# Kernel tuning notes

Hardware: AMD Instinct MI355X
Metric: run time of the kernel (lower is better)

Reference implementation:

```python
import jax, jax.numpy as jnp
import numpy as np

N = 16384      # total atoms (8 proteins x ~2048)
E = 524288     # N * max_neighbors(32)
B = 8          # graphs
F_IN = 26      # 20 residue types + 6 atom types
D = 128        # node_dim
H = 256        # hidden_dim
OUT = 64       # output_dim
L = 4          # n_layers
N_RBF = 16
CUTOFF = 10.0


def setup_inputs() -> dict:
    key = jax.random.key(0)
    ks = jax.random.split(key, 24)
    s = 0.05
    inp = {
        "positions": jax.random.normal(ks[0], (N, 3), jnp.float32) * 10.0,
        "node_features": jax.random.normal(ks[1], (N, F_IN), jnp.float32),
        "edge_index": jax.random.randint(ks[2], (2, E), 0, N, jnp.int32),
        "batch": jnp.sort(jax.random.randint(ks[3], (N,), 0, B, jnp.int32)),
        # node embedding MLP
        "emb_W1": jax.random.normal(ks[4], (F_IN, D), jnp.float32) * s,
        "emb_b1": jnp.zeros((D,), jnp.float32),
        "emb_W2": jax.random.normal(ks[5], (D, D), jnp.float32) * s,
        "emb_b2": jnp.zeros((D,), jnp.float32),
        # per-layer message MLP: [2D + n_rbf] -> H -> D
        "msg_W1": jax.random.normal(ks[6], (L, 2 * D + N_RBF, H), jnp.float32) * s,
        "msg_b1": jnp.zeros((L, H), jnp.float32),
        "msg_W2": jax.random.normal(ks[7], (L, H, D), jnp.float32) * s,
        "msg_b2": jnp.zeros((L, D), jnp.float32),
        # per-layer update MLP: [2D] -> H -> D (residual)
        "upd_W1": jax.random.normal(ks[8], (L, 2 * D, H), jnp.float32) * s,
        "upd_b1": jnp.zeros((L, H), jnp.float32),
        "upd_W2": jax.random.normal(ks[9], (L, H, D), jnp.float32) * s,
        "upd_b2": jnp.zeros((L, D), jnp.float32),
        # readout MLP: D -> H -> OUT
        "r_W1": jax.random.normal(ks[10], (D, H), jnp.float32) * s,
        "r_b1": jnp.zeros((H,), jnp.float32),
        "r_W2": jax.random.normal(ks[11], (H, OUT), jnp.float32) * s,
        "r_b2": jnp.zeros((OUT,), jnp.float32),
    }
    return inp


def _mlp2(x, W1, b1, W2, b2):
    return jax.nn.silu(x @ W1 + b1) @ W2 + b2


def _edge_rbf(positions, src, dst):
    rel = positions[dst] - positions[src]                      # (E,3)
    d = jnp.sqrt(jnp.sum(rel * rel, axis=-1) + 1e-12)          # (E,)
    centers = jnp.linspace(0.0, CUTOFF, N_RBF, dtype=positions.dtype)
    width = CUTOFF / N_RBF
    rbf = jnp.exp(-((d[:, None] - centers) ** 2) / (2.0 * width * width))  # (E,n_rbf)
    env = 0.5 * (jnp.cos(jnp.pi * d / CUTOFF) + 1.0) * (d < CUTOFF)        # cosine cutoff
    return rbf * env[:, None]


def reference(positions, node_features, edge_index, batch,
              emb_W1, emb_b1, emb_W2, emb_b2,
              msg_W1, msg_b1, msg_W2, msg_b2,
              upd_W1, upd_b1, upd_W2, upd_b2,
              r_W1, r_b1, r_W2, r_b2):
    src, dst = edge_index[0], edge_index[1]
    h = _mlp2(node_features, emb_W1, emb_b1, emb_W2, emb_b2)   # (N,D)
    ef = _edge_rbf(positions, src, dst)                        # (E,n_rbf)
    for i in range(L):
        m_in = jnp.concatenate([h[src], h[dst], ef], axis=-1)  # (E,2D+n_rbf)
        m = _mlp2(m_in, msg_W1[i], msg_b1[i], msg_W2[i], msg_b2[i])  # (E,D)
        agg = jax.ops.segment_sum(m, dst, num_segments=N)      # (N,D)
        u_in = jnp.concatenate([h, agg], axis=-1)              # (N,2D)
        h = h + _mlp2(u_in, upd_W1[i], upd_b1[i], upd_W2[i], upd_b2[i])
    # mean readout per graph
    counts = jax.ops.segment_sum(jnp.ones((N,), h.dtype), batch, num_segments=B)
    g = jax.ops.segment_sum(h, batch, num_segments=B) / jnp.maximum(counts, 1.0)[:, None]
    return _mlp2(g, r_W1, r_b1, r_W2, r_b2)                    # (B,OUT)
```

## Files before the change

### kernel.cpp

```cpp
#include <hip/hip_runtime.h>
#include <math.h>

#define NATOMS 16384
#define NEDGES 524288
#define NLAYERS 4
#define TE 64

typedef __bf16 bf16x8 __attribute__((ext_vector_type(8)));
typedef __bf16 bf16x4 __attribute__((ext_vector_type(4)));
typedef __bf16 bf16x2 __attribute__((ext_vector_type(2)));
typedef float f32x4 __attribute__((ext_vector_type(4)));

__device__ __forceinline__ float silu_f(float x) {
  return x * __builtin_amdgcn_rcpf(1.0f + __expf(-x));
}

__global__ __launch_bounds__(1024) void scan_kernel(
    const int* __restrict__ counts, int* __restrict__ cursor,
    float* __restrict__ degf)
{
  __shared__ int s_tot[1024];
  int tid = threadIdx.x;
  int v[16];
  {
    const int4* cp = (const int4*)(counts + tid * 16);
    int4 a = cp[0], b = cp[1], c = cp[2], d = cp[3];
    v[0]=a.x; v[1]=a.y; v[2]=a.z; v[3]=a.w;
    v[4]=b.x; v[5]=b.y; v[6]=b.z; v[7]=b.w;
    v[8]=c.x; v[9]=c.y; v[10]=c.z; v[11]=c.w;
    v[12]=d.x; v[13]=d.y; v[14]=d.z; v[15]=d.w;
  }
  int tot = 0;
  #pragma unroll
  for (int i = 0; i < 16; i++) tot += v[i];
  s_tot[tid] = tot;
  __syncthreads();
  for (int off = 1; off < 1024; off <<= 1) {
    int t = (tid >= off) ? s_tot[tid - off] : 0;
    __syncthreads();
    s_tot[tid] += t;
    __syncthreads();
  }
  int run = s_tot[tid] - tot;
  #pragma unroll
  for (int i = 0; i < 16; i++) {
    cursor[tid * 16 + i] = run;
    degf[tid * 16 + i] = (float)v[i];
    run += v[i];
  }
}

__global__ __launch_bounds__(256) void scatter_rbf_kernel(
    const int* __restrict__ src, const int* __restrict__ dst,
    int* __restrict__ cursor, const float* __restrict__ pos,
    int* __restrict__ esrc, int* __restrict__ edst,
    __bf16* __restrict__ efb)
{
  int e = blockIdx.x * 256 + threadIdx.x;
  int s = src[e], d = dst[e];
  int p = atomicAdd(&cursor[d], 1);
  esrc[p] = s;
  edst[p] = d;
  float dx = pos[d * 3 + 0] - pos[s * 3 + 0];
  float dy = pos[d * 3 + 1] - pos[s * 3 + 1];
  float dz = pos[d * 3 + 2] - pos[s * 3 + 2];
  float dist = sqrtf(dx * dx + dy * dy + dz * dz + 1e-12f);
  float env = (dist < 10.0f)
                  ? 0.5f * (cosf(3.14159265358979f * dist * 0.1f) + 1.0f)
                  : 0.0f;
  bf16x8 o0, o1;
  #pragma unroll
  for (int i = 0; i < 16; i++) {
    float c = (10.0f / 15.0f) * (float)i;
    float t = dist - c;
    float v = env * __expf(-t * t * 1.28f);
    if (i < 8) o0[i] = (__bf16)v; else o1[i - 8] = (__bf16)v;
  }
  *(bf16x8*)(efb + (size_t)p * 16 + 0) = o0;
  *(bf16x8*)(efb + (size_t)p * 16 + 8) = o1;
}

#define NB_PL   50
#define NB_PREP (NB_PL * NLAYERS)
#define NB_HIST (NEDGES / 256)
#define NB_EMB  (NATOMS / 32)

__global__ __launch_bounds__(256) void front_kernel(
    const float* __restrict__ mW1, const float* __restrict__ mW2,
    const float* __restrict__ uW1, const float* __restrict__ uW2,
    const float* __restrict__ mb2,
    __bf16* __restrict__ W1at, __bf16* __restrict__ W1bt,
    __bf16* __restrict__ B2c, __bf16* __restrict__ uW1ft,
    __bf16* __restrict__ uW2t, float* __restrict__ b2u,
    const int* __restrict__ dstI, int* __restrict__ counts,
    const float* __restrict__ x, const float* __restrict__ eW1,
    const float* __restrict__ eb1, const float* __restrict__ eW2,
    const float* __restrict__ eb2, float* __restrict__ h,
    __bf16* __restrict__ hb)
{
  __shared__ __align__(16) char smem[19712];
  int bxf = blockIdx.x, tid = threadIdx.x;

  if (bxf < NB_PREP) {
    int l = bxf / NB_PL;
    int bx = bxf - l * NB_PL;
    if (bx < 16) {
      float (*tile)[65] = (float(*)[65])smem;
      int tt = bx & 7;
      int row0 = ((tt >> 2) * 64) + ((bx < 8) ? 0 : 128);
      int col0 = (tt & 3) * 64;
      const float* Sp = mW1 + (size_t)l * (272 * 256) + (size_t)row0 * 256 + col0;
      __bf16* Dq = ((bx < 8) ? W1at : W1bt) + (size_t)l * (256 * 128);
      int dro = (bx < 8) ? row0 : row0 - 128;
      int c = tid & 63, r4 = tid >> 6;
      #pragma unroll
      for (int i = 0; i < 16; i++)
        tile[r4 + i * 4][c] = Sp[(size_t)(r4 + i * 4) * 256 + c];
      __syncthreads();
      #pragma unroll
      for (int i = 0; i < 16; i++) {
        int dr = r4 + i * 4;
        Dq[(size_t)(col0 + dr) * 128 + dro + c] = (__bf16)tile[c][dr];
      }
    } else if (bx == 16) {
      float (*t3)[257] = (float(*)[257])smem;
      const float* Sp = mW1 + (size_t)l * (272 * 256) + 256 * 256;
      #pragma unroll
      for (int i = 0; i < 16; i++) t3[i][tid] = Sp[i * 256 + tid];
      __syncthreads();
      __bf16* Dp = B2c + (size_t)l * (256 * 32) + (size_t)tid * 32;
      #pragma unroll
      for (int g = 0; g < 4; g++) {
        bf16x8 o;
        #pragma unroll
        for (int j2 = 0; j2 < 8; j2++) {
          int k = g * 8 + j2;
          o[j2] = (__bf16)((k < 16) ? t3[k][tid] : 0.0f);
        }
        *(bf16x8*)(Dp + g * 8) = o;
      }
    } else if (bx < 25) {
      float (*tile)[65] = (float(*)[65])smem;
      int tt = bx - 17;
      int row0 = (tt >> 2) * 64;
      int col0 = (tt & 3) * 64;
      const float* Sp = uW1 + (size_t)l * 65536 + (size_t)row0 * 256 + col0;
      __bf16* Dq = uW1ft + (size_t)l * (256 * 384);
      int c = tid & 63, r4 = tid >> 6;
      #pragma unroll
      for (int i = 0; i < 16; i++)
        tile[r4 + i * 4][c] = Sp[(size_t)(r4 + i * 4) * 256 + c];
      __syncthreads();
      #pragma unroll
      for (int i = 0; i < 16; i++) {
        int dr = r4 + i * 4;
        Dq[(size_t)(col0 + dr) * 384 + row0 + c] = (__bf16)tile[c][dr];
      }
    } else if (bx < 41) {
      float (*sA)[128] = (float(*)[128])smem;
      int r0 = (bx - 25) * 16;
      const float* Ap = mW2 + (size_t)(l * 256 + r0) * 128;
      #pragma unroll
      for (int i = 0; i < 8; i++) {
        int idx = i * 256 + tid;
        ((float*)smem)[idx] = Ap[idx];
      }
      __syncthreads();
      const float* Bp = uW1 + (size_t)l * 65536 + 128 * 256 + tid;
      float acc[16];
      #pragma unroll
      for (int r = 0; r < 16; r++) acc[r] = 0.0f;
      for (int k = 0; k < 128; k++) {
        float b = Bp[(size_t)k * 256];
        #pragma unroll
        for (int r = 0; r < 16; r++) acc[r] += sA[r][k] * b;
      }
      __bf16* Dp = uW1ft + (size_t)l * (256 * 384) + (size_t)tid * 384 + 128 + r0;
      bf16x8 o0, o1;
      #pragma unroll
      for (int r = 0; r < 8; r++) { o0[r] = (__bf16)acc[r]; o1[r] = (__bf16)acc[8 + r]; }
      *(bf16x8*)Dp = o0;
      *(bf16x8*)(Dp + 8) = o1;
    } else if (bx < 49) {
      float (*tile)[65] = (float(*)[65])smem;
      int tt = bx - 41;
      int row0 = (tt >> 1) * 64;
      int col0 = (tt & 1) * 64;
      const float* Sp = uW2 + (size_t)l * (256 * 128) + (size_t)row0 * 128 + col0;
      __bf16* Dq = uW2t + (size_t)l * (128 * 256);
      int c = tid & 63, r4 = tid >> 6;
      #pragma unroll
      for (int i = 0; i < 16; i++)
        tile[r4 + i * 4][c] = Sp[(size_t)(r4 + i * 4) * 128 + c];
      __syncthreads();
      #pragma unroll
      for (int i = 0; i < 16; i++) {
        int dr = r4 + i * 4;
        Dq[(size_t)(col0 + dr) * 256 + row0 + c] = (__bf16)tile[c][dr];
      }
    } else {
      int cc = tid;
      float acc = 0.0f;
      for (int j2 = 0; j2 < 128; j2++)
        acc += mb2[l * 128 + j2] * uW1[(size_t)l * 65536 + (size_t)(128 + j2) * 256 + cc];
      b2u[l * 256 + cc] = acc;
    }
  } else if (bxf < NB_PREP + NB_HIST) {
    int e = (bxf - NB_PREP) * 256 + tid;
    atomicAdd(&counts[dstI[e]], 1);
  } else {
    int nb = bxf - (NB_PREP + NB_HIST);
    int n0e = nb * 32;
    float* xsf = (float*)smem;
    float (*hid2)[128] = (float(*)[128])(smem + 32 * 26 * 4);
    for (int i = tid; i < 32 * 26; i += 256)
      xsf[i] = x[(size_t)n0e * 26 + i];
    __syncthreads();
    int j = tid & 127, ns = tid >> 7;
    float a1[16];
    {
      float bb = eb1[j];
      #pragma unroll
      for (int i = 0; i < 16; i++) a1[i] = bb;
    }
    for (int k = 0; k < 26; k++) {
      float w = eW1[k * 128 + j];
      #pragma unroll
      for (int i = 0; i < 16; i++) a1[i] += xsf[(ns * 16 + i) * 26 + k] * w;
    }
    #pragma unroll
    for (int i = 0; i < 16; i++) hid2[ns * 16 + i][j] = silu_f(a1[i]);
    __syncthreads();
    float a2[16];
    {
      float bb = eb2[j];
      #pragma unroll
      for (int i = 0; i < 16; i++) a2[i] = bb;
    }
    for (int k = 0; k < 128; k++) {
      float w = eW2[k * 128 + j];
      #pragma unroll
      for (int i = 0; i < 16; i++) a2[i] += hid2[ns * 16 + i][k] * w;
    }
    #pragma unroll
    for (int i = 0; i < 16; i++) {
      int n = n0e + ns * 16 + i;
      h[(size_t)n * 128 + j] = a2[i];
      hb[(size_t)n * 128 + j] = (__bf16)a2[i];
    }
  }
}

__global__ __launch_bounds__(256) void zprep_kernel(
    const __bf16* __restrict__ hb, const float* __restrict__ b1,
    const __bf16* __restrict__ W1at, const __bf16* __restrict__ W1bt,
    __bf16* __restrict__ z1b, __bf16* __restrict__ z2b, float* __restrict__ aggH)
{
  __shared__ __bf16 s_n[64][136];
  int tid = threadIdx.x, n0 = blockIdx.x * 64;
  {
    int n = tid >> 2, t4 = tid & 3;
    const bf16x8* hr = (const bf16x8*)(hb + (size_t)(n0 + n) * 128);
    #pragma unroll
    for (int i = 0; i < 4; i++)
      *(bf16x8*)&s_n[n][t4 * 8 + 32 * i] = hr[t4 + 4 * i];
  }
  {
    float4 zz = make_float4(0.f, 0.f, 0.f, 0.f);
    float4* ap = (float4*)(aggH + (size_t)n0 * 256);
    for (int i = tid; i < 64 * 256 / 4; i += 256) ap[i] = zz;
  }
  __syncthreads();
  const int wv = tid >> 6, ln = tid & 63, lc = ln & 15, qd = ln >> 4;
  for (int cp = 0; cp < 2; cp++) {
    f32x4 aA[4][2], aB[4][2];
    #pragma unroll
    for (int nt = 0; nt < 2; nt++) {
      float bv = b1[cp * 128 + wv * 32 + nt * 16 + lc];
      #pragma unroll
      for (int mt = 0; mt < 4; mt++) {
        aA[mt][nt][0] = 0.f; aA[mt][nt][1] = 0.f;
        aA[mt][nt][2] = 0.f; aA[mt][nt][3] = 0.f;
        aB[mt][nt][0] = bv; aB[mt][nt][1] = bv;
        aB[mt][nt][2] = bv; aB[mt][nt][3] = bv;
      }
    }
    #pragma unroll
    for (int kt = 0; kt < 4; kt++) {
      bf16x8 af[4];
      #pragma unroll
      for (int mt = 0; mt < 4; mt++)
        af[mt] = *(const bf16x8*)&s_n[mt * 16 + lc][kt * 32 + qd * 8];
      bf16x8 bwA[2], bwB[2];
      #pragma unroll
      for (int nt = 0; nt < 2; nt++) {
        int c = cp * 128 + wv * 32 + nt * 16 + lc;
        bwA[nt] = *(const bf16x8*)(W1at + (size_t)c * 128 + kt * 32 + qd * 8);
        bwB[nt] = *(const bf16x8*)(W1bt + (size_t)c * 128 + kt * 32 + qd * 8);
      }
      #pragma unroll
      for (int mt = 0; mt < 4; mt++)
        #pragma unroll
        for (int nt = 0; nt < 2; nt++) {
          aA[mt][nt] = __builtin_amdgcn_mfma_f32_16x16x32_bf16(af[mt], bwA[nt], aA[mt][nt], 0, 0, 0);
          aB[mt][nt] = __builtin_amdgcn_mfma_f32_16x16x32_bf16(af[mt], bwB[nt], aB[mt][nt], 0, 0, 0);
        }
    }
    #pragma unroll
    for (int mt = 0; mt < 4; mt++)
      #pragma unroll
      for (int nt = 0; nt < 2; nt++) {
        int c = cp * 128 + wv * 32 + nt * 16 + lc;
        #pragma unroll
        for (int r = 0; r < 4; r++) {
          int n = n0 + mt * 16 + qd * 4 + r;
          z1b[(size_t)n * 256 + c] = (__bf16)aA[mt][nt][r];
          z2b[(size_t)n * 256 + c] = (__bf16)aB[mt][nt][r];
        }
      }
  }
}

__global__ __launch_bounds__(256, 8) void msg_mfma_kernel(
    const __bf16* __restrict__ z1b, const __bf16* __restrict__ z2b,
    const __bf16* __restrict__ efb,
    const int* __restrict__ esrc, const int* __restrict__ edst,
    const __bf16* __restrict__ B2c, float* __restrict__ aggH)
{
  __shared__ __align__(16) __bf16 s_hT[128][68];
  __shared__ __align__(16) __bf16 s_ef[TE][16];
  __shared__ int s_src[TE];
  __shared__ int s_dst[TE];
  __shared__ unsigned int s_mask[2];

  int tid = threadIdx.x;
  const int cpx = (NEDGES / TE) >> 3;
  int wg = (blockIdx.x & 7) * cpx + (blockIdx.x >> 3);
  int e0 = wg * TE;

  if (tid < TE) {
    int d = edst[e0 + tid];
    s_dst[tid] = d;
    int dp = (tid == 0) ? (d ^ 1) : edst[e0 + tid - 1];
    unsigned long long mb = __ballot(d != dp);
    if (tid == 0) { s_mask[0] = (unsigned int)mb; s_mask[1] = (unsigned int)(mb >> 32); }
  } else if (tid < 2 * TE) {
    s_src[tid - TE] = esrc[e0 + tid - TE];
  }
  {
    int e = tid >> 2, t4 = tid & 3;
    if (t4 < 2)
      *(bf16x8*)&s_ef[e][t4 * 8] =
          *(const bf16x8*)(efb + (size_t)(e0 + e) * 16 + t4 * 8);
  }
  __syncthreads();

  const int wv = tid >> 6, ln = tid & 63, lc = ln & 15, qd = ln >> 4;

  bf16x8 bI;
  #pragma unroll
  for (int j = 0; j < 8; j++)
    bI[j] = (__bf16)((lc == (qd & 1) * 8 + j) ? 1.0f : 0.0f);

  const __bf16* pz[4];
  #pragma unroll
  for (int mt = 0; mt < 4; mt++) {
    int m = mt * 16 + lc;
    int row = (qd < 2) ? s_src[m] : s_dst[m];
    pz[mt] = ((qd < 2) ? z1b : z2b) + (size_t)row * 256 + (qd & 1) * 8;
  }

  bf16x8 aef[4];
  #pragma unroll
  for (int mt = 0; mt < 4; mt++)
    aef[mt] = *(const bf16x8*)&s_ef[mt * 16 + lc][(qd & 1) * 8];

  const int sj = tid & 127;
  const int srow0 = (tid >> 7) * 32;
  const unsigned int smask = __builtin_amdgcn_readfirstlane(s_mask[tid >> 7]);

  #pragma unroll
  for (int hf = 0; hf < 2; hf++) {
    if (hf) __syncthreads();

    #pragma unroll
    for (int nt = 0; nt < 2; nt++) {
      const int cb = hf * 128 + wv * 32 + nt * 16;
      bf16x8 bw = *(const bf16x8*)(B2c + (size_t)(cb + lc) * 32 + qd * 8);
      #pragma unroll
      for (int mt = 0; mt < 4; mt++) {
        bf16x8 az = *(const bf16x8*)(pz[mt] + cb);
        f32x4 z; z[0] = 0.f; z[1] = 0.f; z[2] = 0.f; z[3] = 0.f;
        f32x4 acc = __builtin_amdgcn_mfma_f32_16x16x32_bf16(az, bI, z, 0, 0, 0);
        acc = __builtin_amdgcn_mfma_f32_16x16x32_bf16(aef[mt], bw, acc, 0, 0, 0);
        bf16x4 pv;
        pv[0] = (__bf16)silu_f(acc[0]); pv[1] = (__bf16)silu_f(acc[1]);
        pv[2] = (__bf16)silu_f(acc[2]); pv[3] = (__bf16)silu_f(acc[3]);
        *(bf16x4*)&s_hT[wv * 32 + nt * 16 + lc][mt * 16 + qd * 4] = pv;
      }
    }
    __syncthreads();

    {
      const int gcol = hf * 128 + sj;
      float acc = 0.0f;
      int cur = s_dst[srow0];
      #pragma unroll
      for (int i = 0; i < 32; i += 4) {
        unsigned int bm = (smask >> i) & 0xFu;
        if (i == 0) bm &= 0xEu;
        bf16x4 p = *(const bf16x4*)&s_hT[sj][srow0 + i];
        if (bm == 0u) {
          acc += ((float)p[0] + (float)p[1]) + ((float)p[2] + (float)p[3]);
        } else {
          #pragma unroll
          for (int r = 0; r < 4; r++) {
            if ((bm >> r) & 1u) {
              atomicAdd(&aggH[(size_t)cur * 256 + gcol], acc);
              acc = 0.0f; cur = s_dst[srow0 + i + r];
            }
            acc += (float)p[r];
          }
        }
      }
      atomicAdd(&aggH[(size_t)cur * 256 + gcol], acc);
    }
  }
}

__global__ __launch_bounds__(512, 2) void upd_mfma_kernel(
    float* __restrict__ h, __bf16* __restrict__ hb,
    float* __restrict__ aggH, const float* __restrict__ degf,
    const __bf16* __restrict__ uW1ft, const float* __restrict__ b1,
    const float* __restrict__ b2u,
    const __bf16* __restrict__ uW2t, const float* __restrict__ b2,
    int do_z, const float* __restrict__ nb1,
    const __bf16* __restrict__ nW1at, const __bf16* __restrict__ nW1bt,
    __bf16* __restrict__ z1b, __bf16* __restrict__ z2b)
{
  __shared__ __bf16 s_u[64][392];
  __shared__ __bf16 s_uh[64][264];
  int tid = threadIdx.x, n0 = blockIdx.x * 64;
  {
    int n = tid >> 3, t8 = tid & 7;
    const bf16x8* hr = (const bf16x8*)(hb + (size_t)(n0 + n) * 128);
    #pragma unroll
    for (int i = 0; i < 2; i++)
      *(bf16x8*)&s_u[n][t8 * 8 + 64 * i] = hr[t8 + 8 * i];
    const float* sr = aggH + (size_t)(n0 + n) * 256;
    #pragma unroll
    for (int i = 0; i < 4; i++) {
      int col = t8 * 8 + i * 64;
      float4 a = *(const float4*)(sr + col);
      float4 b = *(const float4*)(sr + col + 4);
      bf16x8 o;
      o[0] = (__bf16)a.x; o[1] = (__bf16)a.y; o[2] = (__bf16)a.z; o[3] = (__bf16)a.w;
      o[4] = (__bf16)b.x; o[5] = (__bf16)b.y; o[6] = (__bf16)b.z; o[7] = (__bf16)b.w;
      *(bf16x8*)&s_u[n][128 + col] = o;
    }
  }
  __syncthreads();
  const int wv = tid >> 6, ln = tid & 63, lc = ln & 15, qd = ln >> 4;

  float dg[4][4];
  #pragma unroll
  for (int mt = 0; mt < 4; mt++)
    #pragma unroll
    for (int r = 0; r < 4; r++)
      dg[mt][r] = degf[n0 + mt * 16 + qd * 4 + r];

  {
    f32x4 acc1[4][2];
    #pragma unroll
    for (int nt = 0; nt < 2; nt++) {
      int c = wv * 32 + nt * 16 + lc;
      float bv = b1[c];
      float b2uv = b2u[c];
      #pragma unroll
      for (int mt = 0; mt < 4; mt++)
        #pragma unroll
        for (int r = 0; r < 4; r++)
          acc1[mt][nt][r] = bv + dg[mt][r] * b2uv;
    }
    #pragma unroll
    for (int kt = 0; kt < 12; kt++) {
      bf16x8 af[4];
      #pragma unroll
      for (int mt = 0; mt < 4; mt++)
        af[mt] = *(const bf16x8*)&s_u[mt * 16 + lc][kt * 32 + qd * 8];
      bf16x8 bw[2];
      #pragma unroll
      for (int nt = 0; nt < 2; nt++)
        bw[nt] = *(const bf16x8*)(uW1ft +
                 (size_t)(wv * 32 + nt * 16 + lc) * 384 + kt * 32 + qd * 8);
      #pragma unroll
      for (int mt = 0; mt < 4; mt++)
        #pragma unroll
        for (int nt = 0; nt < 2; nt++)
          acc1[mt][nt] = __builtin_amdgcn_mfma_f32_16x16x32_bf16(af[mt], bw[nt], acc1[mt][nt], 0, 0, 0);
    }
    #pragma unroll
    for (int mt = 0; mt < 4; mt++)
      #pragma unroll
      for (int nt = 0; nt < 2; nt++) {
        int cc = wv * 32 + nt * 16 + lc;
        #pragma unroll
        for (int r = 0; r < 4; r++)
          s_uh[mt * 16 + qd * 4 + r][cc] = (__bf16)silu_f(acc1[mt][nt][r]);
      }
  }
  __syncthreads();

  const int ow = wv * 16 + lc;
  f32x4 acc2[4];
  {
    float bv = b2[ow];
    #pragma unroll
    for (int mt = 0; mt < 4; mt++) {
      acc2[mt][0] = bv; acc2[mt][1] = bv; acc2[mt][2] = bv; acc2[mt][3] = bv;
    }
  }
  #pragma unroll
  for (int kt = 0; kt < 8; kt++) {
    bf16x8 a2[4];
    #pragma unroll
    for (int mt = 0; mt < 4; mt++)
      a2[mt] = *(const bf16x8*)&s_uh[mt * 16 + lc][kt * 32 + qd * 8];
    bf16x8 b2w = *(const bf16x8*)(uW2t + (size_t)ow * 256 + kt * 32 + qd * 8);
    #pragma unroll
    for (int mt = 0; mt < 4; mt++)
      acc2[mt] = __builtin_amdgcn_mfma_f32_16x16x32_bf16(a2[mt], b2w, acc2[mt], 0, 0, 0);
  }

  #pragma unroll
  for (int mt = 0; mt < 4; mt++)
    #pragma unroll
    for (int r = 0; r < 4; r++) {
      int n = n0 + mt * 16 + qd * 4 + r;
      float v = h[(size_t)n * 128 + ow] + acc2[mt][r];
      h[(size_t)n * 128 + ow] = v;
      hb[(size_t)n * 128 + ow] = (__bf16)v;
    }

  if (do_z) {
    __syncthreads();
    {
      float4 zz = make_float4(0.f, 0.f, 0.f, 0.f);
      float4* ap = (float4*)(aggH + (size_t)n0 * 256);
      for (int i = tid; i < 64 * 256 / 4; i += 512) ap[i] = zz;
      int n = tid >> 3, t8 = tid & 7;
      const bf16x8* hr = (const bf16x8*)(hb + (size_t)(n0 + n) * 128);
      #pragma unroll
      for (int i = 0; i < 2; i++)
        *(bf16x8*)&s_u[n][t8 * 8 + 64 * i] = hr[t8 + 8 * i];
    }
    __syncthreads();
    f32x4 aA[4][2], aB[4][2];
    #pragma unroll
    for (int nt = 0; nt < 2; nt++) {
      float bv = nb1[wv * 32 + nt * 16 + lc];
      #pragma unroll
      for (int mt = 0; mt < 4; mt++) {
        aA[mt][nt][0] = 0.f; aA[mt][nt][1] = 0.f;
        aA[mt][nt][2] = 0.f; aA[mt][nt][3] = 0.f;
        aB[mt][nt][0] = bv; aB[mt][nt][1] = bv;
        aB[mt][nt][2] = bv; aB[mt][nt][3] = bv;
      }
    }
    #pragma unroll
    for (int kt = 0; kt < 4; kt++) {
      bf16x8 af[4];
      #pragma unroll
      for (int mt = 0; mt < 4; mt++)
        af[mt] = *(const bf16x8*)&s_u[mt * 16 + lc][kt * 32 + qd * 8];
      bf16x8 bwA[2], bwB[2];
      #pragma unroll
      for (int nt = 0; nt < 2; nt++) {
        int c = wv * 32 + nt * 16 + lc;
        bwA[nt] = *(const bf16x8*)(nW1at + (size_t)c * 128 + kt * 32 + qd * 8);
        bwB[nt] = *(const bf16x8*)(nW1bt + (size_t)c * 128 + kt * 32 + qd * 8);
      }
      #pragma unroll
      for (int mt = 0; mt < 4; mt++)
        #pragma unroll
        for (int nt = 0; nt < 2; nt++) {
          aA[mt][nt] = __builtin_amdgcn_mfma_f32_16x16x32_bf16(af[mt], bwA[nt], aA[mt][nt], 0, 0, 0);
          aB[mt][nt] = __builtin_amdgcn_mfma_f32_16x16x32_bf16(af[mt], bwB[nt], aB[mt][nt], 0, 0, 0);
        }
    }
    #pragma unroll
    for (int mt = 0; mt < 4; mt++)
      #pragma unroll
      for (int nt = 0; nt < 2; nt++) {
        int c = wv * 32 + nt * 16 + lc;
        #pragma unroll
        for (int r = 0; r < 4; r++) {
          int n = n0 + mt * 16 + qd * 4 + r;
          z1b[(size_t)n * 256 + c] = (__bf16)aA[mt][nt][r];
          z2b[(size_t)n * 256 + c] = (__bf16)aB[mt][nt][r];
        }
      }
  }
}

__global__ __launch_bounds__(128) void readout_sum_kernel(
    const float* __restrict__ h, const int* __restrict__ batch,
    float* __restrict__ gsum, float* __restrict__ gcnt)
{
  int j = threadIdx.x;
  int n0 = blockIdx.x * 128;
  float acc = 0.f, cacc = 0.f;
  int cur = batch[n0];
  for (int i = 0; i < 128; i++) {
    int b = batch[n0 + i];
    if (b != cur) {
      atomicAdd(&gsum[cur * 128 + j], acc);
      if (j == 0) atomicAdd(&gcnt[cur], cacc);
      acc = 0.f; cacc = 0.f; cur = b;
    }
    acc += h[(size_t)(n0 + i) * 128 + j];
    cacc += 1.f;
  }
  atomicAdd(&gsum[cur * 128 + j], acc);
  if (j == 0) atomicAdd(&gcnt[cur], cacc);
}

__global__ __launch_bounds__(256) void readout_mlp_kernel(
    const float* __restrict__ gsum, const float* __restrict__ gcnt,
    const float* __restrict__ W1, const float* __restrict__ b1,
    const float* __restrict__ W2, const float* __restrict__ b2,
    float* __restrict__ out)
{
  __shared__ float g[8][128];
  __shared__ float hid[8][256];
  int tid = threadIdx.x;
  for (int i = tid; i < 8 * 128; i += 256) {
    int b = i >> 7, c = i & 127;
    g[b][c] = gsum[i] / fmaxf(gcnt[b], 1.0f);
  }
  __syncthreads();
  {
    float bb = b1[tid];
    float a[8];
    #pragma unroll
    for (int b = 0; b < 8; b++) a[b] = bb;
    for (int k = 0; k < 128; k++) {
      float w = W1[k * 256 + tid];
      #pragma unroll
      for (int b = 0; b < 8; b++) a[b] += g[b][k] * w;
    }
    #pragma unroll
    for (int b = 0; b < 8; b++) hid[b][tid] = silu_f(a[b]);
  }
  __syncthreads();
  int j = tid & 63, bg = tid >> 6;
  float a0 = b2[j], a1 = b2[j];
  for (int k = 0; k < 256; k++) {
    float w = W2[k * 64 + j];
    a0 += hid[bg * 2 + 0][k] * w;
    a1 += hid[bg * 2 + 1][k] * w;
  }
  out[(bg * 2 + 0) * 64 + j] = a0;
  out[(bg * 2 + 1) * 64 + j] = a1;
}

extern "C" void kernel_launch(void* const* d_in, const int* in_sizes, int n_in,
                              void* d_out, int out_size, void* d_ws, size_t ws_size,
                              hipStream_t stream) {
  const float* pos   = (const float*)d_in[0];
  const float* xfeat = (const float*)d_in[1];
  const int*   eidx  = (const int*)d_in[2];
  const int*   batch = (const int*)d_in[3];
  const float* eW1 = (const float*)d_in[4];
  const float* eb1 = (const float*)d_in[5];
  const float* eW2 = (const float*)d_in[6];
  const float* eb2 = (const float*)d_in[7];
  const float* mW1 = (const float*)d_in[8];
  const float* mb1 = (const float*)d_in[9];
  const float* mW2 = (const float*)d_in[10];
  const float* mb2 = (const float*)d_in[11];
  const float* uW1 = (const float*)d_in[12];
  const float* ub1 = (const float*)d_in[13];
  const float* uW2 = (const float*)d_in[14];
  const float* ub2 = (const float*)d_in[15];
  const float* rW1 = (const float*)d_in[16];
  const float* rb1 = (const float*)d_in[17];
  const float* rW2 = (const float*)d_in[18];
  const float* rb2 = (const float*)d_in[19];

  const int* srcI = eidx;
  const int* dstI = eidx + NEDGES;

  char* base = (char*)d_ws;
  float* h    = (float*)base;  base += (size_t)NATOMS * 128 * 4;
  float* aggH = (float*)base;  base += (size_t)NATOMS * 256 * 4;
  __bf16* z1b = (__bf16*)base; base += (size_t)NATOMS * 256 * 2;
  __bf16* z2b = (__bf16*)base; base += (size_t)NATOMS * 256 * 2;
  __bf16* hb  = (__bf16*)base; base += (size_t)NATOMS * 128 * 2;
  __bf16* efb = (__bf16*)base; base += (size_t)NEDGES * 16 * 2;
  __bf16* W1at = (__bf16*)base; base += (size_t)NLAYERS * 256 * 128 * 2;
  __bf16* W1bt = (__bf16*)base; base += (size_t)NLAYERS * 256 * 128 * 2;
  __bf16* B2c  = (__bf16*)base; base += (size_t)NLAYERS * 256 * 32 * 2;
  __bf16* uW1ft = (__bf16*)base; base += (size_t)NLAYERS * 256 * 384 * 2;
  __bf16* uW2t = (__bf16*)base; base += (size_t)NLAYERS * 128 * 256 * 2;
  float* b2u  = (float*)base;  base += (size_t)NLAYERS * 256 * 4;
  float* degf = (float*)base;  base += (size_t)NATOMS * 4;
  float* gsum = (float*)base;  base += 8 * 128 * 4;
  float* gcnt = (float*)base;  base += 8 * 4;
  int* counts = (int*)base;    base += (size_t)NATOMS * 4;
  int* cursor = (int*)base;    base += (size_t)NATOMS * 4;
  int* esrc   = (int*)base;    base += (size_t)NEDGES * 4;
  int* edst   = (int*)base;    base += (size_t)NEDGES * 4;

  hipMemsetAsync(counts, 0, NATOMS * sizeof(int), stream);

  front_kernel<<<NB_PREP + NB_HIST + NB_EMB, 256, 0, stream>>>(
      mW1, mW2, uW1, uW2, mb2, W1at, W1bt, B2c, uW1ft, uW2t, b2u,
      dstI, counts, xfeat, eW1, eb1, eW2, eb2, h, hb);

  scan_kernel<<<1, 1024, 0, stream>>>(counts, cursor, degf);
  scatter_rbf_kernel<<<NEDGES / 256, 256, 0, stream>>>(
      srcI, dstI, cursor, pos, esrc, edst, efb);

  zprep_kernel<<<NATOMS / 64, 256, 0, stream>>>(
      hb, mb1, W1at, W1bt, z1b, z2b, aggH);

  for (int l = 0; l < NLAYERS; l++) {
    int ln = (l < NLAYERS - 1) ? (l + 1) : l;
    msg_mfma_kernel<<<NEDGES / TE, 256, 0, stream>>>(
        z1b, z2b, efb, esrc, edst,
        B2c + (size_t)l * 256 * 32, aggH);
    upd_mfma_kernel<<<NATOMS / 64, 512, 0, stream>>>(
        h, hb, aggH, degf,
        uW1ft + (size_t)l * 256 * 384, ub1 + (size_t)l * 256,
        b2u + (size_t)l * 256,
        uW2t + (size_t)l * 128 * 256, ub2 + (size_t)l * 128,
        (l < NLAYERS - 1) ? 1 : 0,
        mb1 + (size_t)ln * 256,
        W1at + (size_t)ln * 256 * 128, W1bt + (size_t)ln * 256 * 128,
        z1b, z2b);
  }

  hipMemsetAsync(gsum, 0, (8 * 128 + 8) * sizeof(float), stream);
  readout_sum_kernel<<<NATOMS / 128, 128, 0, stream>>>(h, batch, gsum, gcnt);
  readout_mlp_kernel<<<1, 256, 0, stream>>>(gsum, gcnt, rW1, rb1, rW2, rb2,
                                            (float*)d_out);
}
```

Measured before the change: 582.9 us.

## Merge scatter and zprep kernels, fold gsum memset, use wave-shuffle scan

The edge scatter/RBF kernel and the z-projection prep kernel become one launch with block ranges split by blockIdx, and the readout accumulator memset moves into an extra block of the front kernel. The single-block prefix scan now uses wave shuffles plus a small per-wave shared array instead of a 1024-step shared-memory loop with barriers. The aim is to cut launch count and per-launch gaps and to speed up the serial scan. The merged kernel mixes two kinds of blocks with different resource needs, and the shared-memory allocation for the z-prep path now applies to the scatter blocks as well.

```diff
diff --git a/kernel.cpp b/kernel.cpp
--- a/kernel.cpp
+++ b/kernel.cpp
@@ -19,7 +19,7 @@
     const int* __restrict__ counts, int* __restrict__ cursor,
     float* __restrict__ degf)
 {
-  __shared__ int s_tot[1024];
+  __shared__ int s_ws[16];
   int tid = threadIdx.x;
   int v[16];
   {
@@ -33,51 +33,34 @@
   int tot = 0;
   #pragma unroll
   for (int i = 0; i < 16; i++) tot += v[i];
-  s_tot[tid] = tot;
+
+  int lane = tid & 63, wv = tid >> 6;
+  int sc = tot;
+  #pragma unroll
+  for (int off = 1; off < 64; off <<= 1) {
+    int t = __shfl_up(sc, off, 64);
+    if (lane >= off) sc += t;
+  }
+  if (lane == 63) s_ws[wv] = sc;
   __syncthreads();
-  for (int off = 1; off < 1024; off <<= 1) {
-    int t = (tid >= off) ? s_tot[tid - off] : 0;
-    __syncthreads();
-    s_tot[tid] += t;
-    __syncthreads();
-  }
-  int run = s_tot[tid] - tot;
+  if (wv == 0 && lane < 16) {
+    int w = s_ws[lane];
+    #pragma unroll
+    for (int off = 1; off < 16; off <<= 1) {
+      int t = __shfl_up(w, off, 64);
+      if (lane >= off) w += t;
+    }
+    s_ws[lane] = w;
+  }
+  __syncthreads();
+  int wbase = (wv == 0) ? 0 : s_ws[wv - 1];
+  int run = wbase + sc - tot;
   #pragma unroll
   for (int i = 0; i < 16; i++) {
     cursor[tid * 16 + i] = run;
     degf[tid * 16 + i] = (float)v[i];
     run += v[i];
   }
-}
-
-__global__ __launch_bounds__(256) void scatter_rbf_kernel(
-    const int* __restrict__ src, const int* __restrict__ dst,
-    int* __restrict__ cursor, const float* __restrict__ pos,
-    int* __restrict__ esrc, int* __restrict__ edst,
-    __bf16* __restrict__ efb)
-{
-  int e = blockIdx.x * 256 + threadIdx.x;
-  int s = src[e], d = dst[e];
-  int p = atomicAdd(&cursor[d], 1);
-  esrc[p] = s;
-  edst[p] = d;
-  float dx = pos[d * 3 + 0] - pos[s * 3 + 0];
-  float dy = pos[d * 3 + 1] - pos[s * 3 + 1];
-  float dz = pos[d * 3 + 2] - pos[s * 3 + 2];
-  float dist = sqrtf(dx * dx + dy * dy + dz * dz + 1e-12f);
-  float env = (dist < 10.0f)
-                  ? 0.5f * (cosf(3.14159265358979f * dist * 0.1f) + 1.0f)
-                  : 0.0f;
-  bf16x8 o0, o1;
-  #pragma unroll
-  for (int i = 0; i < 16; i++) {
-    float c = (10.0f / 15.0f) * (float)i;
-    float t = dist - c;
-    float v = env * __expf(-t * t * 1.28f);
-    if (i < 8) o0[i] = (__bf16)v; else o1[i - 8] = (__bf16)v;
-  }
-  *(bf16x8*)(efb + (size_t)p * 16 + 0) = o0;
-  *(bf16x8*)(efb + (size_t)p * 16 + 8) = o1;
 }
 
 #define NB_PL   50
@@ -96,7 +79,7 @@
     const float* __restrict__ x, const float* __restrict__ eW1,
     const float* __restrict__ eb1, const float* __restrict__ eW2,
     const float* __restrict__ eb2, float* __restrict__ h,
-    __bf16* __restrict__ hb)
+    __bf16* __restrict__ hb, float* __restrict__ gsum)
 {
   __shared__ __align__(16) char smem[19712];
   int bxf = blockIdx.x, tid = threadIdx.x;
@@ -208,7 +191,7 @@
   } else if (bxf < NB_PREP + NB_HIST) {
     int e = (bxf - NB_PREP) * 256 + tid;
     atomicAdd(&counts[dstI[e]], 1);
-  } else {
+  } else if (bxf < NB_PREP + NB_HIST + NB_EMB) {
     int nb = bxf - (NB_PREP + NB_HIST);
     int n0e = nb * 32;
     float* xsf = (float*)smem;
@@ -248,16 +231,53 @@
       h[(size_t)n * 128 + j] = a2[i];
       hb[(size_t)n * 128 + j] = (__bf16)a2[i];
     }
-  }
-}
-
-__global__ __launch_bounds__(256) void zprep_kernel(
+  } else {
+    for (int i = tid; i < 8 * 128 + 8; i += 256) gsum[i] = 0.0f;
+  }
+}
+
+#define NB_SCAT (NEDGES / 256)
+
+__global__ __launch_bounds__(256) void prep2_kernel(
+    const int* __restrict__ src, const int* __restrict__ dst,
+    int* __restrict__ cursor, const float* __restrict__ pos,
+    int* __restrict__ esrc, int* __restrict__ edst,
+    __bf16* __restrict__ efb,
     const __bf16* __restrict__ hb, const float* __restrict__ b1,
     const __bf16* __restrict__ W1at, const __bf16* __restrict__ W1bt,
-    __bf16* __restrict__ z1b, __bf16* __restrict__ z2b, float* __restrict__ aggH)
+    __bf16* __restrict__ z1b, __bf16* __restrict__ z2b,
+    float* __restrict__ aggH)
 {
   __shared__ __bf16 s_n[64][136];
-  int tid = threadIdx.x, n0 = blockIdx.x * 64;
+  int tid = threadIdx.x;
+
+  if (blockIdx.x < NB_SCAT) {
+    int e = blockIdx.x * 256 + tid;
+    int s = src[e], d = dst[e];
+    int p = atomicAdd(&cursor[d], 1);
+    esrc[p] = s;
+    edst[p] = d;
+    float dx = pos[d * 3 + 0] - pos[s * 3 + 0];
+    float dy = pos[d * 3 + 1] - pos[s * 3 + 1];
+    float dz = pos[d * 3 + 2] - pos[s * 3 + 2];
+    float dist = sqrtf(dx * dx + dy * dy + dz * dz + 1e-12f);
+    float env = (dist < 10.0f)
+                    ? 0.5f * (cosf(3.14159265358979f * dist * 0.1f) + 1.0f)
+                    : 0.0f;
+    bf16x8 o0, o1;
+    #pragma unroll
+    for (int i = 0; i < 16; i++) {
+      float c = (10.0f / 15.0f) * (float)i;
+      float t = dist - c;
+      float v = env * __expf(-t * t * 1.28f);
+      if (i < 8) o0[i] = (__bf16)v; else o1[i - 8] = (__bf16)v;
+    }
+    *(bf16x8*)(efb + (size_t)p * 16 + 0) = o0;
+    *(bf16x8*)(efb + (size_t)p * 16 + 8) = o1;
+    return;
+  }
+
+  int n0 = (blockIdx.x - NB_SCAT) * 64;
   {
     int n = tid >> 2, t4 = tid & 3;
     const bf16x8* hr = (const bf16x8*)(hb + (size_t)(n0 + n) * 128);
@@ -714,15 +734,14 @@
 
   hipMemsetAsync(counts, 0, NATOMS * sizeof(int), stream);
 
-  front_kernel<<<NB_PREP + NB_HIST + NB_EMB, 256, 0, stream>>>(
+  front_kernel<<<NB_PREP + NB_HIST + NB_EMB + 1, 256, 0, stream>>>(
       mW1, mW2, uW1, uW2, mb2, W1at, W1bt, B2c, uW1ft, uW2t, b2u,
-      dstI, counts, xfeat, eW1, eb1, eW2, eb2, h, hb);
+      dstI, counts, xfeat, eW1, eb1, eW2, eb2, h, hb, gsum);
 
   scan_kernel<<<1, 1024, 0, stream>>>(counts, cursor, degf);
-  scatter_rbf_kernel<<<NEDGES / 256, 256, 0, stream>>>(
-      srcI, dstI, cursor, pos, esrc, edst, efb);
-
-  zprep_kernel<<<NATOMS / 64, 256, 0, stream>>>(
+
+  prep2_kernel<<<NB_SCAT + NATOMS / 64, 256, 0, stream>>>(
+      srcI, dstI, cursor, pos, esrc, edst, efb,
       hb, mb1, W1at, W1bt, z1b, z2b, aggH);
 
   for (int l = 0; l < NLAYERS; l++) {
@@ -741,7 +760,6 @@
         z1b, z2b);
   }
 
-  hipMemsetAsync(gsum, 0, (8 * 128 + 8) * sizeof(float), stream);
   readout_sum_kernel<<<NATOMS / 128, 128, 0, stream>>>(h, batch, gsum, gcnt);
   readout_mlp_kernel<<<1, 256, 0, stream>>>(gsum, gcnt, rW1, rb1, rW2, rb2,
                                             (float*)d_out);
```

Measured after the change: 572.4 us. No clear change (-1.8%).
